# Kernel tuning notes

Measured on AMD Instinct MI355X. Metric: run time of the kernel, lower is better.

Reference implementation:

```python
import jax, jax.numpy as jnp
import numpy as np

N = 8192
D = 512


def setup_inputs() -> dict:
    key = jax.random.key(0)
    ks = jax.random.split(key, 7)
    X = jax.random.normal(ks[0], (N, D), dtype=jnp.float32)
    adj = jax.random.randint(ks[1], (N, N), 0, 2, dtype=jnp.int32)
    # guarantee at least one neighbor per row (self-loop) so softmax is defined
    adj = adj.at[jnp.arange(N), jnp.arange(N)].set(1)
    s = 1.0 / np.sqrt(D)
    Wq = jax.random.normal(ks[2], (D, D), dtype=jnp.float32) * s
    Wk = jax.random.normal(ks[3], (D, D), dtype=jnp.float32) * s
    Wv = jax.random.normal(ks[4], (D, D), dtype=jnp.float32) * s
    Wo = jax.random.normal(ks[5], (D, D), dtype=jnp.float32) * s
    bo = jnp.zeros((D,), dtype=jnp.float32)
    return {"X": X, "adj": adj, "Wq": Wq, "Wk": Wk, "Wv": Wv, "Wo": Wo, "bo": bo}


def reference(X, adj, Wq, Wk, Wv, Wo, bo):
    # torch Linear(no bias): y = x @ W.T
    Q = X @ Wq.T                                  # [N, D]
    K = X @ Wk.T                                  # [N, D]
    V = X @ Wv.T                                  # [N, D]
    scale = 1.0 / jnp.sqrt(jnp.asarray(D, X.dtype))
    scores = jnp.einsum('nd,md->nm', Q, K) * scale  # [N, N]
    scores = jnp.where(adj == 0, -jnp.inf, scores)
    attn = jax.nn.softmax(scores, axis=-1)          # [N, N]
    out = attn @ V                                  # [N, D]
    out = out @ Wo.T + bo                           # [N, D]
    return out
```

## Files before the change

kernel.cpp:

```cpp
#include <hip/hip_runtime.h>

namespace {

constexpr int NR = 8192;
constexpr int DD = 512;
constexpr int NSPLIT = 4;
constexpr int KVLEN = NR / NSPLIT;
constexpr int KT = 32;
constexpr int NT = KVLEN / KT;
constexpr int QB = 64;
constexpr float SCALE = 0.04419417382415922f;

typedef __bf16 bf16x8 __attribute__((ext_vector_type(8)));
typedef __bf16 bf16x4 __attribute__((ext_vector_type(4)));
typedef float  f32x16 __attribute__((ext_vector_type(16)));
typedef float  f32x4  __attribute__((ext_vector_type(4)));

__device__ __forceinline__ f32x16 mfma32(bf16x8 a, bf16x8 b, f32x16 c) {
    return __builtin_amdgcn_mfma_f32_32x32x16_bf16(a, b, c, 0, 0, 0);
}
__device__ __forceinline__ f32x4 mfma16(bf16x8 a, bf16x8 b, f32x4 c) {
    return __builtin_amdgcn_mfma_f32_16x16x32_bf16(a, b, c, 0, 0, 0);
}

typedef const __attribute__((address_space(1))) void g_void;
typedef __attribute__((address_space(3))) void l_void;
__device__ __forceinline__ void lds_dma16(const void* g, void* l) {
    __builtin_amdgcn_global_load_lds((g_void*)g, (l_void*)l, 16, 0, 0);
}

__device__ __forceinline__ bf16x8 cvt8(float4 a, float4 b) {
    bf16x8 o;
    o[0] = (__bf16)a.x; o[1] = (__bf16)a.y; o[2] = (__bf16)a.z; o[3] = (__bf16)a.w;
    o[4] = (__bf16)b.x; o[5] = (__bf16)b.y; o[6] = (__bf16)b.z; o[7] = (__bf16)b.w;
    return o;
}

__device__ __forceinline__ size_t kfa(int n, int d) {
    int tile = n >> 5, kv = n & 31;
    int chunk = (d >> 3) ^ (kv & 7);
    return (size_t)tile * 16384 + kv * 512 + chunk * 8 + (d & 7);
}
__device__ __forceinline__ size_t vfa(int n, int d) {
    size_t chunk = (size_t)(((n >> 5) * 4 + (d >> 7)) * 8 +
                            ((d >> 6) & 1) * 4 + ((d >> 5) & 1) * 2 + ((n >> 4) & 1));
    return chunk * 512 + ((((n >> 3) & 1) * 32 + (d & 31)) * 8) + (n & 7);
}

__global__ void __launch_bounds__(256)
bitpack_kernel(const int* __restrict__ adj, unsigned* __restrict__ abits) {
    const int w = threadIdx.x >> 6, lane = threadIdx.x & 63;
    const int q = blockIdx.x * 4 + w;
    const int* row = adj + (size_t)q * NR;
    unsigned* orow = abits + (size_t)q * 256;
    for (int i = 0; i < 128; ++i) {
        unsigned long long m = __ballot(row[i * 64 + lane] != 0);
        if (lane == 0) { orow[2 * i] = (unsigned)m; orow[2 * i + 1] = (unsigned)(m >> 32); }
    }
}

template<bool FINAL>
__global__ void __launch_bounds__(256, 2)
gemm_kernel(const float* __restrict__ Xf, const __bf16* __restrict__ Aop,
            const float* __restrict__ B0, const float* __restrict__ B1,
            const float* __restrict__ B2,
            __bf16* __restrict__ C0, __bf16* __restrict__ C1, __bf16* __restrict__ C2,
            const float* __restrict__ bias, float* __restrict__ Cf,
            const float* __restrict__ lsum)
{
    const float* B = B0;
    __bf16* Cb = C0;
    int mode = 0;
    if (!FINAL) {
        if (blockIdx.y == 1)      { B = B1; Cb = C1; mode = 1; }
        else if (blockIdx.y == 2) { B = B2; Cb = C2; }
    }
    __shared__ __bf16 As[128][72];
    __shared__ __bf16 Bs[128][72];
    const int t = threadIdx.x;
    const int w = t >> 6, lane = t & 63, lo = lane & 31, hi = lane >> 5;
    const int wm = w >> 1, wn = w & 1;
    const int bm = (blockIdx.x >> 2) * 128;
    const int bn = (blockIdx.x & 3) * 128;

    f32x16 acc[2][2];
    #pragma unroll
    for (int a = 0; a < 2; ++a)
        #pragma unroll
        for (int b = 0; b < 2; ++b)
            #pragma unroll
            for (int r = 0; r < 16; ++r) acc[a][b][r] = 0.f;

    for (int k0 = 0; k0 < DD; k0 += 64) {
        __syncthreads();
        #pragma unroll
        for (int pp = 0; pp < 2; ++pp) {
            int r = pp * 64 + (t >> 2), c = (t & 3) * 16;
            if (FINAL) {
                int row = bm + r;
                float l0 = lsum[row], l1 = lsum[NR + row],
                      l2 = lsum[2 * NR + row], l3 = lsum[3 * NR + row];
                float Winv = 1.f / (l0 + l1 + l2 + l3);
                float w0 = l0 * Winv, w1 = l1 * Winv, w2 = l2 * Winv, w3 = l3 * Winv;
                const size_t stride = (size_t)NR * DD;
                #pragma unroll
                for (int cc = 0; cc < 2; ++cc) {
                    const size_t base = (size_t)row * DD + k0 + c + cc * 8;
                    bf16x8 o0 = *(const bf16x8*)(Aop + base);
                    bf16x8 o1 = *(const bf16x8*)(Aop + stride + base);
                    bf16x8 o2 = *(const bf16x8*)(Aop + 2 * stride + base);
                    bf16x8 o3 = *(const bf16x8*)(Aop + 3 * stride + base);
                    bf16x8 om;
                    #pragma unroll
                    for (int e = 0; e < 8; ++e)
                        om[e] = (__bf16)(w0 * (float)o0[e] + w1 * (float)o1[e] +
                                         w2 * (float)o2[e] + w3 * (float)o3[e]);
                    *(bf16x8*)&As[r][c + cc * 8] = om;
                }
            } else {
                const float* asrc = Xf + (size_t)(bm + r) * DD + k0 + c;
                float4 a0 = *(const float4*)(asrc);
                float4 a1 = *(const float4*)(asrc + 4);
                float4 a2 = *(const float4*)(asrc + 8);
                float4 a3 = *(const float4*)(asrc + 12);
                *(bf16x8*)&As[r][c]     = cvt8(a0, a1);
                *(bf16x8*)&As[r][c + 8] = cvt8(a2, a3);
            }
            const float* bsrc = B + (size_t)(bn + r) * DD + k0 + c;
            float4 b0 = *(const float4*)(bsrc);
            float4 b1 = *(const float4*)(bsrc + 4);
            float4 b2 = *(const float4*)(bsrc + 8);
            float4 b3 = *(const float4*)(bsrc + 12);
            *(bf16x8*)&Bs[r][c]     = cvt8(b0, b1);
            *(bf16x8*)&Bs[r][c + 8] = cvt8(b2, b3);
        }
        __syncthreads();
        #pragma unroll
        for (int ks = 0; ks < 4; ++ks) {
            bf16x8 a0 = *(const bf16x8*)&As[wm * 64 + lo][ks * 16 + hi * 8];
            bf16x8 a1 = *(const bf16x8*)&As[wm * 64 + 32 + lo][ks * 16 + hi * 8];
            bf16x8 b0 = *(const bf16x8*)&Bs[wn * 64 + lo][ks * 16 + hi * 8];
            bf16x8 b1 = *(const bf16x8*)&Bs[wn * 64 + 32 + lo][ks * 16 + hi * 8];
            acc[0][0] = mfma32(a0, b0, acc[0][0]);
            acc[0][1] = mfma32(a0, b1, acc[0][1]);
            acc[1][0] = mfma32(a1, b0, acc[1][0]);
            acc[1][1] = mfma32(a1, b1, acc[1][1]);
        }
    }
    #pragma unroll
    for (int mi = 0; mi < 2; ++mi)
        #pragma unroll
        for (int ni = 0; ni < 2; ++ni) {
            int col = bn + wn * 64 + ni * 32 + lo;
            float bv = 0.f;
            if (FINAL) bv = bias[col];
            #pragma unroll
            for (int r = 0; r < 16; ++r) {
                int row = bm + wm * 64 + mi * 32 + (r & 3) + 8 * (r >> 2) + 4 * hi;
                if (FINAL) {
                    Cf[(size_t)row * DD + col] = acc[mi][ni][r] + bv;
                } else {
                    size_t a = (mode == 1) ? kfa(row, col) : ((size_t)row * DD + col);
                    Cb[a] = (__bf16)acc[mi][ni][r];
                }
            }
        }
}

__global__ void __launch_bounds__(256)
repack_v(const __bf16* __restrict__ V, __bf16* __restrict__ VF) {
    __shared__ __bf16 tile[64][72];
    const int t = threadIdx.x;
    const int rb = blockIdx.x * 64;
    const int cb = blockIdx.y * 64;
    #pragma unroll
    for (int pp = 0; pp < 2; ++pp) {
        int r = pp * 32 + (t >> 3), c = (t & 7) * 8;
        *(bf16x8*)&tile[r][c] = *(const bf16x8*)(V + (size_t)(rb + r) * DD + cb + c);
    }
    __syncthreads();
    #pragma unroll
    for (int pp = 0; pp < 2; ++pp) {
        int vid = pp * 256 + t;
        int oct = vid >> 6;
        int dd = vid & 63;
        bf16x8 o;
        #pragma unroll
        for (int e = 0; e < 8; ++e) o[e] = tile[oct * 8 + e][dd];
        *(bf16x8*)(VF + vfa(rb + oct * 8, cb + dd)) = o;
    }
}

__global__ void __launch_bounds__(256, 2)
flash_kernel(const __bf16* __restrict__ Qg, const __bf16* __restrict__ KF,
             const __bf16* __restrict__ VF, const unsigned* __restrict__ abits,
             __bf16* __restrict__ Opart, float* __restrict__ lsum_g)
{
    __shared__ __bf16 Klds[2][16384];
    __shared__ __bf16 Pl[2][QB][40];
    __shared__ float  ll[QB];

    const int t = threadIdx.x;
    const int w = t >> 6, lane = t & 63;
    const int lo = lane & 31, hi = lane >> 5;
    const int l15 = lane & 15, G = lane >> 4;
    const int bid = blockIdx.x;
    const int xcd = bid & 7;
    const int split = xcd >> 1;
    const int qblk = (((xcd & 1) << 6) | (bid >> 3)) * QB;
    const int kv0 = split * KVLEN;
    const int tile0 = kv0 >> 5;

    bf16x8 qa[16];
    #pragma unroll
    for (int ks = 0; ks < 16; ++ks)
        qa[ks] = *(const bf16x8*)(Qg + (size_t)(qblk + w * 16 + l15) * DD + ks * 32 + G * 8);

    f32x16 O[2][2][2];
    #pragma unroll
    for (int h = 0; h < 2; ++h)
        #pragma unroll
        for (int a = 0; a < 2; ++a)
            #pragma unroll
            for (int b = 0; b < 2; ++b)
                #pragma unroll
                for (int r = 0; r < 16; ++r) O[h][a][b][r] = 0.f;

    const unsigned* abp = abits + (size_t)(qblk + w * 16 + l15) * 256 + tile0;
    unsigned wcur = abp[0];
    float l_run = 0.f;
    const int hsw = l15 & 7;

    #pragma unroll
    for (int i = 0; i < 8; ++i)
        lds_dma16(KF + (size_t)tile0 * 16384 + w * 4096 + i * 512 + lane * 8,
                  &Klds[0][w * 4096 + i * 512]);
    asm volatile("s_waitcnt vmcnt(0)" ::: "memory");
    __syncthreads();

    {
        #pragma unroll
        for (int i = 0; i < 8; ++i)
            lds_dma16(KF + (size_t)(tile0 + 1) * 16384 + w * 4096 + i * 512 + lane * 8,
                      &Klds[1][w * 4096 + i * 512]);
        f32x4 St0, St1;
        #pragma unroll
        for (int r = 0; r < 4; ++r) { St0[r] = 0.f; St1[r] = 0.f; }
        #pragma unroll
        for (int ks = 0; ks < 16; ++ks) {
            int csw = (((ks * 4 + G) ^ hsw) << 3);
            bf16x8 k0 = *(const bf16x8*)&Klds[0][l15 * 512 + csw];
            bf16x8 k1 = *(const bf16x8*)&Klds[0][(16 + l15) * 512 + csw];
            St0 = mfma16(k0, qa[ks], St0);
            St1 = mfma16(k1, qa[ks], St1);
        }
        float l_add = 0.f;
        bf16x4 p0v, p1v;
        #pragma unroll
        for (int r = 0; r < 4; ++r) {
            float pv0 = ((wcur >> (G * 4 + r)) & 1u) ? __expf(St0[r] * SCALE) : 0.f;
            float pv1 = ((wcur >> (16 + G * 4 + r)) & 1u) ? __expf(St1[r] * SCALE) : 0.f;
            l_add += pv0 + pv1;
            p0v[r] = (__bf16)pv0; p1v[r] = (__bf16)pv1;
        }
        *(bf16x4*)&Pl[0][w * 16 + l15][G * 4]      = p0v;
        *(bf16x4*)&Pl[0][w * 16 + l15][16 + G * 4] = p1v;
        float a = l_add + __shfl_xor(l_add, 16);
        a += __shfl_xor(a, 32);
        l_run += a;
        unsigned wnxt = abp[1];
        asm volatile("s_waitcnt vmcnt(1) lgkmcnt(0)" ::: "memory");
        asm volatile("s_barrier" ::: "memory");
        wcur = wnxt;
    }

    for (int tl = 1; tl < NT; ++tl) {
        const int b = tl & 1;
        const int tn = (tl + 1 == NT) ? 0 : tl + 1;

        const __bf16* vf = VF + (size_t)((tile0 + tl - 1) * 4 + w) * 4096;
        bf16x8 vb[8];
        #pragma unroll
        for (int i = 0; i < 8; ++i)
            vb[i] = *(const bf16x8*)(vf + i * 512 + lane * 8);
        bf16x8 pa[2][2];
        #pragma unroll
        for (int mi = 0; mi < 2; ++mi)
            #pragma unroll
            for (int ksp = 0; ksp < 2; ++ksp)
                pa[mi][ksp] = *(const bf16x8*)&Pl[b ^ 1][mi * 32 + lo][ksp * 16 + hi * 8];
        #pragma unroll
        for (int i = 0; i < 8; ++i)
            lds_dma16(KF + (size_t)(tile0 + tn) * 16384 + w * 4096 + i * 512 + lane * 8,
                      &Klds[b ^ 1][w * 4096 + i * 512]);

        __builtin_amdgcn_s_setprio(1);
        f32x4 St0, St1;
        #pragma unroll
        for (int r = 0; r < 4; ++r) { St0[r] = 0.f; St1[r] = 0.f; }
        #pragma unroll
        for (int ks = 0; ks < 16; ++ks) {
            int csw = (((ks * 4 + G) ^ hsw) << 3);
            bf16x8 k0 = *(const bf16x8*)&Klds[b][l15 * 512 + csw];
            bf16x8 k1 = *(const bf16x8*)&Klds[b][(16 + l15) * 512 + csw];
            St0 = mfma16(k0, qa[ks], St0);
            St1 = mfma16(k1, qa[ks], St1);
        }
        #pragma unroll
        for (int h = 0; h < 2; ++h)
            #pragma unroll
            for (int ni = 0; ni < 2; ++ni) {
                O[h][0][ni] = mfma32(pa[0][0], vb[h * 4 + ni * 2 + 0], O[h][0][ni]);
                O[h][1][ni] = mfma32(pa[1][0], vb[h * 4 + ni * 2 + 0], O[h][1][ni]);
                O[h][0][ni] = mfma32(pa[0][1], vb[h * 4 + ni * 2 + 1], O[h][0][ni]);
                O[h][1][ni] = mfma32(pa[1][1], vb[h * 4 + ni * 2 + 1], O[h][1][ni]);
            }
        __builtin_amdgcn_s_setprio(0);

        {
            float l_add = 0.f;
            bf16x4 p0v, p1v;
            #pragma unroll
            for (int r = 0; r < 4; ++r) {
                float pv0 = ((wcur >> (G * 4 + r)) & 1u) ? __expf(St0[r] * SCALE) : 0.f;
                float pv1 = ((wcur >> (16 + G * 4 + r)) & 1u) ? __expf(St1[r] * SCALE) : 0.f;
                l_add += pv0 + pv1;
                p0v[r] = (__bf16)pv0; p1v[r] = (__bf16)pv1;
            }
            *(bf16x4*)&Pl[b][w * 16 + l15][G * 4]      = p0v;
            *(bf16x4*)&Pl[b][w * 16 + l15][16 + G * 4] = p1v;
            float a = l_add + __shfl_xor(l_add, 16);
            a += __shfl_xor(a, 32);
            l_run += a;
        }
        unsigned wnxt = abp[tn];
        asm volatile("s_waitcnt vmcnt(1) lgkmcnt(0)" ::: "memory");
        asm volatile("s_barrier" ::: "memory");
        wcur = wnxt;
    }
    {
        const int b = (NT - 1) & 1;
        bf16x8 pa[2][2];
        #pragma unroll
        for (int mi = 0; mi < 2; ++mi)
            #pragma unroll
            for (int ksp = 0; ksp < 2; ++ksp)
                pa[mi][ksp] = *(const bf16x8*)&Pl[b][mi * 32 + lo][ksp * 16 + hi * 8];
        const __bf16* vf = VF + (size_t)((tile0 + NT - 1) * 4 + w) * 4096;
        #pragma unroll
        for (int h = 0; h < 2; ++h)
            #pragma unroll
            for (int ni = 0; ni < 2; ++ni) {
                bf16x8 vb0 = *(const bf16x8*)(vf + (h * 4 + ni * 2 + 0) * 512 + lane * 8);
                bf16x8 vb1 = *(const bf16x8*)(vf + (h * 4 + ni * 2 + 1) * 512 + lane * 8);
                O[h][0][ni] = mfma32(pa[0][0], vb0, O[h][0][ni]);
                O[h][1][ni] = mfma32(pa[1][0], vb0, O[h][1][ni]);
                O[h][0][ni] = mfma32(pa[0][1], vb1, O[h][0][ni]);
                O[h][1][ni] = mfma32(pa[1][1], vb1, O[h][1][ni]);
            }
    }
    if (lane < 16) {
        ll[w * 16 + lane] = l_run;
        lsum_g[(size_t)split * NR + qblk + w * 16 + lane] = l_run;
    }
    __syncthreads();
    #pragma unroll
    for (int mi = 0; mi < 2; ++mi)
        #pragma unroll
        for (int g = 0; g < 4; ++g) {
            float4 lv = *(const float4*)&ll[mi * 32 + 8 * g + 4 * hi];
            #pragma unroll
            for (int j = 0; j < 4; ++j) {
                float lval = (&lv.x)[j];
                float inv = (lval > 0.f) ? 1.f / lval : 0.f;
                int row = qblk + mi * 32 + 8 * g + 4 * hi + j;
                #pragma unroll
                for (int h = 0; h < 2; ++h)
                    #pragma unroll
                    for (int ni = 0; ni < 2; ++ni) {
                        int col = w * 128 + h * 64 + ni * 32 + lo;
                        Opart[(size_t)split * NR * DD + (size_t)row * DD + col] =
                            (__bf16)(O[h][mi][ni][g * 4 + j] * inv);
                    }
            }
        }
}

}

extern "C" void kernel_launch(void* const* d_in, const int* in_sizes, int n_in,
                              void* d_out, int out_size, void* d_ws, size_t ws_size,
                              hipStream_t stream)
{
    (void)in_sizes; (void)n_in; (void)out_size; (void)ws_size;
    const float* X  = (const float*)d_in[0];
    const int*   adj = (const int*)d_in[1];
    const float* Wq = (const float*)d_in[2];
    const float* Wk = (const float*)d_in[3];
    const float* Wv = (const float*)d_in[4];
    const float* Wo = (const float*)d_in[5];
    const float* bo = (const float*)d_in[6];
    float* out = (float*)d_out;

    char* ws = (char*)d_ws;
    __bf16* Qb   = (__bf16*)(ws + 0);
    __bf16* KFb  = (__bf16*)(ws + 8388608);
    __bf16* VFb  = (__bf16*)(ws + 16777216);
    unsigned* abits = (unsigned*)(ws + 25165824);
    __bf16* Vb   = (__bf16*)(ws + 33554432);
    __bf16* Op   = (__bf16*)(ws + 33554432);
    float*  lseb = (float*)(ws + 67108864);

    bitpack_kernel<<<2048, 256, 0, stream>>>(adj, abits);
    gemm_kernel<false><<<dim3(256, 3), 256, 0, stream>>>(X, nullptr, Wq, Wk, Wv,
                                                         Qb, KFb, Vb,
                                                         nullptr, nullptr, nullptr);
    repack_v<<<dim3(128, 8), 256, 0, stream>>>(Vb, VFb);
    flash_kernel<<<512, 256, 0, stream>>>(Qb, KFb, VFb, abits, Op, lseb);
    gemm_kernel<true><<<dim3(256, 1), 256, 0, stream>>>(nullptr, Op, Wo, nullptr, nullptr,
                                                        nullptr, nullptr, nullptr,
                                                        bo, out, lseb);
}
```

Measured before the change: 430.7 us.

## Halve flash query block, single-buffer K in LDS, raise occupancy to three blocks

Shrinks the query block from 64 to 32 rows and doubles the grid, so each wave now computes one 16x32 score tile and four output accumulators instead of eight. K moves from a double buffer to a single LDS buffer, with an extra barrier before the next tile's DMA, and V loads are split into two halves to reduce live registers. Launch bounds go to 3 blocks per CU. The goal is more parallelism and latency hiding. In exchange, each K/V tile is reused across fewer queries, so global K/V traffic doubles, and the single K buffer adds serialization between score compute and prefetch.

```diff
diff --git a/kernel.cpp b/kernel.cpp
--- a/kernel.cpp
+++ b/kernel.cpp
@@ -8,7 +8,7 @@
 constexpr int KVLEN = NR / NSPLIT;
 constexpr int KT = 32;
 constexpr int NT = KVLEN / KT;
-constexpr int QB = 64;
+constexpr int QB = 32;
 constexpr float SCALE = 0.04419417382415922f;
 
 typedef __bf16 bf16x8 __attribute__((ext_vector_type(8)));
@@ -191,199 +191,188 @@
     }
 }
 
-__global__ void __launch_bounds__(256, 2)
+__global__ void __launch_bounds__(256, 3)
 flash_kernel(const __bf16* __restrict__ Qg, const __bf16* __restrict__ KF,
              const __bf16* __restrict__ VF, const unsigned* __restrict__ abits,
              __bf16* __restrict__ Opart, float* __restrict__ lsum_g)
 {
-    __shared__ __bf16 Klds[2][16384];
+    __shared__ __bf16 Klds[16384];
     __shared__ __bf16 Pl[2][QB][40];
-    __shared__ float  ll[QB];
+    __shared__ float  llp[2][QB];
+    __shared__ float  lls[QB];
 
     const int t = threadIdx.x;
     const int w = t >> 6, lane = t & 63;
     const int lo = lane & 31, hi = lane >> 5;
     const int l15 = lane & 15, G = lane >> 4;
+    const int g = w & 1, h = w >> 1;
     const int bid = blockIdx.x;
     const int xcd = bid & 7;
     const int split = xcd >> 1;
-    const int qblk = (((xcd & 1) << 6) | (bid >> 3)) * QB;
+    const int qblk = (((xcd & 1) << 7) | (bid >> 3)) * QB;
     const int kv0 = split * KVLEN;
     const int tile0 = kv0 >> 5;
 
     bf16x8 qa[16];
     #pragma unroll
     for (int ks = 0; ks < 16; ++ks)
-        qa[ks] = *(const bf16x8*)(Qg + (size_t)(qblk + w * 16 + l15) * DD + ks * 32 + G * 8);
-
-    f32x16 O[2][2][2];
-    #pragma unroll
-    for (int h = 0; h < 2; ++h)
-        #pragma unroll
-        for (int a = 0; a < 2; ++a)
-            #pragma unroll
-            for (int b = 0; b < 2; ++b)
-                #pragma unroll
-                for (int r = 0; r < 16; ++r) O[h][a][b][r] = 0.f;
-
-    const unsigned* abp = abits + (size_t)(qblk + w * 16 + l15) * 256 + tile0;
+        qa[ks] = *(const bf16x8*)(Qg + (size_t)(qblk + g * 16 + l15) * DD + ks * 32 + G * 8);
+
+    f32x16 O[4];
+    #pragma unroll
+    for (int j = 0; j < 4; ++j)
+        #pragma unroll
+        for (int r = 0; r < 16; ++r) O[j][r] = 0.f;
+
+    const unsigned* abp = abits + (size_t)(qblk + g * 16 + l15) * 256 + tile0;
     unsigned wcur = abp[0];
     float l_run = 0.f;
     const int hsw = l15 & 7;
+    const int krow = (h * 16 + l15) * 512;
 
     #pragma unroll
     for (int i = 0; i < 8; ++i)
         lds_dma16(KF + (size_t)tile0 * 16384 + w * 4096 + i * 512 + lane * 8,
-                  &Klds[0][w * 4096 + i * 512]);
+                  &Klds[w * 4096 + i * 512]);
     asm volatile("s_waitcnt vmcnt(0)" ::: "memory");
     __syncthreads();
 
     {
+        f32x4 St;
+        #pragma unroll
+        for (int r = 0; r < 4; ++r) St[r] = 0.f;
+        #pragma unroll
+        for (int ks = 0; ks < 16; ++ks) {
+            int csw = (((ks * 4 + G) ^ hsw) << 3);
+            bf16x8 k = *(const bf16x8*)&Klds[krow + csw];
+            St = mfma16(k, qa[ks], St);
+        }
+        asm volatile("s_waitcnt lgkmcnt(0)" ::: "memory");
+        asm volatile("s_barrier" ::: "memory");
         #pragma unroll
         for (int i = 0; i < 8; ++i)
             lds_dma16(KF + (size_t)(tile0 + 1) * 16384 + w * 4096 + i * 512 + lane * 8,
-                      &Klds[1][w * 4096 + i * 512]);
-        f32x4 St0, St1;
-        #pragma unroll
-        for (int r = 0; r < 4; ++r) { St0[r] = 0.f; St1[r] = 0.f; }
-        #pragma unroll
-        for (int ks = 0; ks < 16; ++ks) {
-            int csw = (((ks * 4 + G) ^ hsw) << 3);
-            bf16x8 k0 = *(const bf16x8*)&Klds[0][l15 * 512 + csw];
-            bf16x8 k1 = *(const bf16x8*)&Klds[0][(16 + l15) * 512 + csw];
-            St0 = mfma16(k0, qa[ks], St0);
-            St1 = mfma16(k1, qa[ks], St1);
-        }
+                      &Klds[w * 4096 + i * 512]);
         float l_add = 0.f;
-        bf16x4 p0v, p1v;
+        bf16x4 pv;
         #pragma unroll
         for (int r = 0; r < 4; ++r) {
-            float pv0 = ((wcur >> (G * 4 + r)) & 1u) ? __expf(St0[r] * SCALE) : 0.f;
-            float pv1 = ((wcur >> (16 + G * 4 + r)) & 1u) ? __expf(St1[r] * SCALE) : 0.f;
-            l_add += pv0 + pv1;
-            p0v[r] = (__bf16)pv0; p1v[r] = (__bf16)pv1;
-        }
-        *(bf16x4*)&Pl[0][w * 16 + l15][G * 4]      = p0v;
-        *(bf16x4*)&Pl[0][w * 16 + l15][16 + G * 4] = p1v;
+            float p = ((wcur >> (h * 16 + G * 4 + r)) & 1u) ? __expf(St[r] * SCALE) : 0.f;
+            l_add += p;
+            pv[r] = (__bf16)p;
+        }
+        *(bf16x4*)&Pl[0][g * 16 + l15][h * 16 + G * 4] = pv;
         float a = l_add + __shfl_xor(l_add, 16);
         a += __shfl_xor(a, 32);
         l_run += a;
-        unsigned wnxt = abp[1];
+        unsigned wn = abp[1];
         asm volatile("s_waitcnt vmcnt(1) lgkmcnt(0)" ::: "memory");
         asm volatile("s_barrier" ::: "memory");
-        wcur = wnxt;
+        wcur = wn;
     }
 
     for (int tl = 1; tl < NT; ++tl) {
         const int b = tl & 1;
         const int tn = (tl + 1 == NT) ? 0 : tl + 1;
 
+        f32x4 St;
+        #pragma unroll
+        for (int r = 0; r < 4; ++r) St[r] = 0.f;
+        #pragma unroll
+        for (int ks = 0; ks < 16; ++ks) {
+            int csw = (((ks * 4 + G) ^ hsw) << 3);
+            bf16x8 k = *(const bf16x8*)&Klds[krow + csw];
+            St = mfma16(k, qa[ks], St);
+        }
+        asm volatile("s_waitcnt lgkmcnt(0)" ::: "memory");
+        asm volatile("s_barrier" ::: "memory");
+
         const __bf16* vf = VF + (size_t)((tile0 + tl - 1) * 4 + w) * 4096;
-        bf16x8 vb[8];
-        #pragma unroll
-        for (int i = 0; i < 8; ++i)
-            vb[i] = *(const bf16x8*)(vf + i * 512 + lane * 8);
-        bf16x8 pa[2][2];
-        #pragma unroll
-        for (int mi = 0; mi < 2; ++mi)
-            #pragma unroll
-            for (int ksp = 0; ksp < 2; ++ksp)
-                pa[mi][ksp] = *(const bf16x8*)&Pl[b ^ 1][mi * 32 + lo][ksp * 16 + hi * 8];
+        bf16x8 vbA0 = *(const bf16x8*)(vf + 0 * 512 + lane * 8);
+        bf16x8 vbA1 = *(const bf16x8*)(vf + 1 * 512 + lane * 8);
+        bf16x8 vbA2 = *(const bf16x8*)(vf + 2 * 512 + lane * 8);
+        bf16x8 vbA3 = *(const bf16x8*)(vf + 3 * 512 + lane * 8);
+        asm volatile("" ::: "memory");
         #pragma unroll
         for (int i = 0; i < 8; ++i)
             lds_dma16(KF + (size_t)(tile0 + tn) * 16384 + w * 4096 + i * 512 + lane * 8,
-                      &Klds[b ^ 1][w * 4096 + i * 512]);
-
-        __builtin_amdgcn_s_setprio(1);
-        f32x4 St0, St1;
-        #pragma unroll
-        for (int r = 0; r < 4; ++r) { St0[r] = 0.f; St1[r] = 0.f; }
-        #pragma unroll
-        for (int ks = 0; ks < 16; ++ks) {
-            int csw = (((ks * 4 + G) ^ hsw) << 3);
-            bf16x8 k0 = *(const bf16x8*)&Klds[b][l15 * 512 + csw];
-            bf16x8 k1 = *(const bf16x8*)&Klds[b][(16 + l15) * 512 + csw];
-            St0 = mfma16(k0, qa[ks], St0);
-            St1 = mfma16(k1, qa[ks], St1);
-        }
-        #pragma unroll
-        for (int h = 0; h < 2; ++h)
-            #pragma unroll
-            for (int ni = 0; ni < 2; ++ni) {
-                O[h][0][ni] = mfma32(pa[0][0], vb[h * 4 + ni * 2 + 0], O[h][0][ni]);
-                O[h][1][ni] = mfma32(pa[1][0], vb[h * 4 + ni * 2 + 0], O[h][1][ni]);
-                O[h][0][ni] = mfma32(pa[0][1], vb[h * 4 + ni * 2 + 1], O[h][0][ni]);
-                O[h][1][ni] = mfma32(pa[1][1], vb[h * 4 + ni * 2 + 1], O[h][1][ni]);
-            }
-        __builtin_amdgcn_s_setprio(0);
-
+                      &Klds[w * 4096 + i * 512]);
         {
             float l_add = 0.f;
-            bf16x4 p0v, p1v;
+            bf16x4 pv;
             #pragma unroll
             for (int r = 0; r < 4; ++r) {
-                float pv0 = ((wcur >> (G * 4 + r)) & 1u) ? __expf(St0[r] * SCALE) : 0.f;
-                float pv1 = ((wcur >> (16 + G * 4 + r)) & 1u) ? __expf(St1[r] * SCALE) : 0.f;
-                l_add += pv0 + pv1;
-                p0v[r] = (__bf16)pv0; p1v[r] = (__bf16)pv1;
+                float p = ((wcur >> (h * 16 + G * 4 + r)) & 1u) ? __expf(St[r] * SCALE) : 0.f;
+                l_add += p;
+                pv[r] = (__bf16)p;
             }
-            *(bf16x4*)&Pl[b][w * 16 + l15][G * 4]      = p0v;
-            *(bf16x4*)&Pl[b][w * 16 + l15][16 + G * 4] = p1v;
+            *(bf16x4*)&Pl[b][g * 16 + l15][h * 16 + G * 4] = pv;
             float a = l_add + __shfl_xor(l_add, 16);
             a += __shfl_xor(a, 32);
             l_run += a;
         }
-        unsigned wnxt = abp[tn];
+        bf16x8 pa0 = *(const bf16x8*)&Pl[b ^ 1][lo][hi * 8];
+        bf16x8 pa1 = *(const bf16x8*)&Pl[b ^ 1][lo][16 + hi * 8];
+        __builtin_amdgcn_s_setprio(1);
+        O[0] = mfma32(pa0, vbA0, O[0]);
+        O[0] = mfma32(pa1, vbA1, O[0]);
+        O[1] = mfma32(pa0, vbA2, O[1]);
+        O[1] = mfma32(pa1, vbA3, O[1]);
+        __builtin_amdgcn_s_setprio(0);
+        asm volatile("" ::: "memory");
+        bf16x8 vbB0 = *(const bf16x8*)(vf + 4 * 512 + lane * 8);
+        bf16x8 vbB1 = *(const bf16x8*)(vf + 5 * 512 + lane * 8);
+        bf16x8 vbB2 = *(const bf16x8*)(vf + 6 * 512 + lane * 8);
+        bf16x8 vbB3 = *(const bf16x8*)(vf + 7 * 512 + lane * 8);
+        __builtin_amdgcn_s_setprio(1);
+        O[2] = mfma32(pa0, vbB0, O[2]);
+        O[2] = mfma32(pa1, vbB1, O[2]);
+        O[3] = mfma32(pa0, vbB2, O[3]);
+        O[3] = mfma32(pa1, vbB3, O[3]);
+        __builtin_amdgcn_s_setprio(0);
+        unsigned wn = abp[tn];
         asm volatile("s_waitcnt vmcnt(1) lgkmcnt(0)" ::: "memory");
         asm volatile("s_barrier" ::: "memory");
-        wcur = wnxt;
-    }
+        wcur = wn;
+    }
+
     {
         const int b = (NT - 1) & 1;
-        bf16x8 pa[2][2];
-        #pragma unroll
-        for (int mi = 0; mi < 2; ++mi)
-            #pragma unroll
-            for (int ksp = 0; ksp < 2; ++ksp)
-                pa[mi][ksp] = *(const bf16x8*)&Pl[b][mi * 32 + lo][ksp * 16 + hi * 8];
+        bf16x8 pa0 = *(const bf16x8*)&Pl[b][lo][hi * 8];
+        bf16x8 pa1 = *(const bf16x8*)&Pl[b][lo][16 + hi * 8];
         const __bf16* vf = VF + (size_t)((tile0 + NT - 1) * 4 + w) * 4096;
         #pragma unroll
-        for (int h = 0; h < 2; ++h)
-            #pragma unroll
-            for (int ni = 0; ni < 2; ++ni) {
-                bf16x8 vb0 = *(const bf16x8*)(vf + (h * 4 + ni * 2 + 0) * 512 + lane * 8);
-                bf16x8 vb1 = *(const bf16x8*)(vf + (h * 4 + ni * 2 + 1) * 512 + lane * 8);
-                O[h][0][ni] = mfma32(pa[0][0], vb0, O[h][0][ni]);
-                O[h][1][ni] = mfma32(pa[1][0], vb0, O[h][1][ni]);
-                O[h][0][ni] = mfma32(pa[0][1], vb1, O[h][0][ni]);
-                O[h][1][ni] = mfma32(pa[1][1], vb1, O[h][1][ni]);
-            }
-    }
-    if (lane < 16) {
-        ll[w * 16 + lane] = l_run;
-        lsum_g[(size_t)split * NR + qblk + w * 16 + lane] = l_run;
-    }
+        for (int j = 0; j < 4; ++j) {
+            bf16x8 v0 = *(const bf16x8*)(vf + (j * 2 + 0) * 512 + lane * 8);
+            bf16x8 v1 = *(const bf16x8*)(vf + (j * 2 + 1) * 512 + lane * 8);
+            O[j] = mfma32(pa0, v0, O[j]);
+            O[j] = mfma32(pa1, v1, O[j]);
+        }
+    }
+    if (lane < 16) llp[h][g * 16 + lane] = l_run;
     __syncthreads();
-    #pragma unroll
-    for (int mi = 0; mi < 2; ++mi)
-        #pragma unroll
-        for (int g = 0; g < 4; ++g) {
-            float4 lv = *(const float4*)&ll[mi * 32 + 8 * g + 4 * hi];
+    if (t < QB) {
+        float s = llp[0][t] + llp[1][t];
+        lls[t] = s;
+        lsum_g[(size_t)split * NR + qblk + t] = s;
+    }
+    __syncthreads();
+    #pragma unroll
+    for (int g4 = 0; g4 < 4; ++g4) {
+        float4 lv = *(const float4*)&lls[g4 * 8 + 4 * hi];
+        #pragma unroll
+        for (int e = 0; e < 4; ++e) {
+            float lval = (&lv.x)[e];
+            float inv = (lval > 0.f) ? 1.f / lval : 0.f;
+            int row = qblk + g4 * 8 + 4 * hi + e;
             #pragma unroll
             for (int j = 0; j < 4; ++j) {
-                float lval = (&lv.x)[j];
-                float inv = (lval > 0.f) ? 1.f / lval : 0.f;
-                int row = qblk + mi * 32 + 8 * g + 4 * hi + j;
-                #pragma unroll
-                for (int h = 0; h < 2; ++h)
-                    #pragma unroll
-                    for (int ni = 0; ni < 2; ++ni) {
-                        int col = w * 128 + h * 64 + ni * 32 + lo;
-                        Opart[(size_t)split * NR * DD + (size_t)row * DD + col] =
-                            (__bf16)(O[h][mi][ni][g * 4 + j] * inv);
-                    }
+                int col = w * 128 + j * 32 + lo;
+                Opart[(size_t)split * NR * DD + (size_t)row * DD + col] =
+                    (__bf16)(O[j][g4 * 4 + e] * inv);
             }
         }
+    }
 }
 
 }
@@ -416,7 +405,7 @@
                                                          Qb, KFb, Vb,
                                                          nullptr, nullptr, nullptr);
     repack_v<<<dim3(128, 8), 256, 0, stream>>>(Vb, VFb);
-    flash_kernel<<<512, 256, 0, stream>>>(Qb, KFb, VFb, abits, Op, lseb);
+    flash_kernel<<<1024, 256, 0, stream>>>(Qb, KFb, VFb, abits, Op, lseb);
     gemm_kernel<true><<<dim3(256, 1), 256, 0, stream>>>(nullptr, Op, Wo, nullptr, nullptr,
                                                         nullptr, nullptr, nullptr,
                                                         bo, out, lseb);
```

New measurement: 920.8 us. 114% more time.
